# Optimization experiments

Measured on AMD Instinct MI355X. Metric: run time of the kernel, lower is better.

Reference implementation:

```python
import math
import jax, jax.numpy as jnp
import numpy as np

B, N, C, H = 64, 197, 768, 12
KEEP_RATE = 0.7

def setup_inputs() -> dict:
    key = jax.random.key(0)
    k0, k1, k2 = jax.random.split(key, 3)
    x = jax.random.normal(k0, (B, N, C), jnp.float32)
    qkv_w = jax.random.normal(k1, (C, 3 * C), jnp.float32) * 0.02
    qkv_b = jnp.zeros((3 * C,), jnp.float32)
    proj_w = jax.random.normal(k2, (C, C), jnp.float32) * 0.02
    proj_b = jnp.zeros((C,), jnp.float32)
    return {"x": x, "qkv_w": qkv_w, "qkv_b": qkv_b, "proj_w": proj_w, "proj_b": proj_b}

def reference(x, qkv_w, qkv_b, proj_w, proj_b):
    b, n, c = x.shape
    d = c // H
    scale = d ** -0.5
    # qkv: [B,N,3C] -> [3,B,H,N,d]
    qkv = (x @ qkv_w + qkv_b).reshape(b, n, 3, H, d)
    qkv = jnp.transpose(qkv, (2, 0, 3, 1, 4))
    q, k, v = qkv[0], qkv[1], qkv[2]
    attn = jax.nn.softmax(jnp.einsum('bhnd,bhmd->bhnm', q, k) * scale, axis=-1)  # [B,H,N,N]
    out = jnp.einsum('bhnm,bhmd->bhnd', attn, v)          # [B,H,N,d]
    out = jnp.transpose(out, (0, 2, 1, 3)).reshape(b, n, c)
    x_out = out @ proj_w + proj_b                          # [B,N,C]
    # dynamic token pruning via CLS attention (row 0, excluding CLS itself)
    left_tokens = math.ceil(KEEP_RATE * (n - 1))
    cls_attn = attn[:, :, 0, 1:].mean(axis=1)              # [B,N-1]
    _, idx = jax.lax.top_k(cls_attn, left_tokens)          # descending, sorted
    index = jnp.broadcast_to(idx[:, :, None], (b, left_tokens, c))
    return (x_out, index, idx, cls_attn, left_tokens)
```

## Files before the change

kernel.cpp:

```cpp
#include <hip/hip_runtime.h>
#include <math.h>

#define BB   64
#define NTOK 197
#define CC   768
#define HH   12
#define DH   64
#define MTOT (BB * NTOK)
#define MPAD 12672
#define LEFT 138

#define XOUT_OFF  0
#define INDEX_OFF 9682944
#define IDX_OFF   16465920
#define CLS_OFF   16474752
#define LT_OFF    16487296

typedef short s8v __attribute__((ext_vector_type(8)));
typedef short s4v __attribute__((ext_vector_type(4)));
typedef float f4v __attribute__((ext_vector_type(4)));

#define GLOAD16(g, l) __builtin_amdgcn_global_load_lds( \
    (const __attribute__((address_space(1))) unsigned int*)(g), \
    (__attribute__((address_space(3))) unsigned int*)(l), 16, 0, 0)

__device__ __forceinline__ unsigned short f2bf(float f) {
    union { float f; unsigned int i; } x; x.f = f;
    unsigned int r = x.i + 0x7FFFu + ((x.i >> 16) & 1u);
    return (unsigned short)(r >> 16);
}

__global__ __launch_bounds__(256)
void convert_x(const float* __restrict__ in, unsigned short* __restrict__ outb)
{
    size_t i = ((size_t)blockIdx.x * 256 + threadIdx.x) * 8;
    float4 a = *(const float4*)(in + i);
    float4 b = *(const float4*)(in + i + 4);
    s8v r;
    r[0] = (short)f2bf(a.x); r[1] = (short)f2bf(a.y);
    r[2] = (short)f2bf(a.z); r[3] = (short)f2bf(a.w);
    r[4] = (short)f2bf(b.x); r[5] = (short)f2bf(b.y);
    r[6] = (short)f2bf(b.z); r[7] = (short)f2bf(b.w);
    *(s8v*)(outb + i) = r;
}

__global__ __launch_bounds__(256)
void transpose_w2(const float* __restrict__ inq, const float* __restrict__ inp,
                  unsigned short* __restrict__ outq, unsigned short* __restrict__ outp)
{
    __shared__ float tile[32][33];
    const int bi = blockIdx.x;
    int bj = blockIdx.y;
    const float* in; unsigned short* outb; int N;
    if (bj < 72) { in = inq; outb = outq; N = 2304; }
    else         { bj -= 72; in = inp; outb = outp; N = 768; }
    const int tx = threadIdx.x & 31, ty = threadIdx.x >> 5;
#pragma unroll
    for (int r = ty; r < 32; r += 8)
        tile[r][tx] = in[(size_t)(bi * 32 + r) * N + bj * 32 + tx];
    __syncthreads();
#pragma unroll
    for (int r = ty; r < 32; r += 8)
        outb[(size_t)(bj * 32 + r) * 768 + bi * 32 + tx] = f2bf(tile[tx][r]);
}

__global__ __launch_bounds__(256, 3)
void gemm_bf16(const unsigned short* __restrict__ A, const unsigned short* __restrict__ BT,
               const float* __restrict__ bias, int ncolt, int mode,
               unsigned short* __restrict__ outb, float* __restrict__ outf)
{
    const int id = blockIdx.x;
    const int xcd = id & 7;
    const int t = id >> 3;
    const int ct = t % ncolt, s = t / ncolt;
    const int rt = s * 8 + xcd;
    if (rt >= 99) return;
    const int m0 = rt * 128, n0 = ct * 128;

    const int tid = threadIdx.x;
    const int wave = tid >> 6, lane = tid & 63;
    const int quad = lane >> 4, l16 = lane & 15;
    const int rowbase = (wave >> 1) * 64, colbase = (wave & 1) * 64;
    __shared__ __align__(16) short As[128 * 64];
    __shared__ __align__(16) short Bs[128 * 64];

    const int rA   = lane >> 3;
    const int gcol = ((lane & 7) ^ rA) * 8;
    unsigned int agof[4], bgof[4];
#pragma unroll
    for (int i = 0; i < 4; ++i) {
        int c = wave * 4 + i;
        agof[i] = (unsigned int)((m0 + c * 8 + rA) * 768 + gcol);
        bgof[i] = (unsigned int)((n0 + c * 8 + rA) * 768 + gcol);
    }
    int aoff[4], boff[4];
#pragma unroll
    for (int i = 0; i < 4; ++i) {
        aoff[i] = (rowbase + i * 16 + l16) * 64 + ((quad ^ (l16 & 7)) * 8);
        boff[i] = (colbase + i * 16 + l16) * 64 + ((quad ^ (l16 & 7)) * 8);
    }

    f4v acc[4][4];
#pragma unroll
    for (int i = 0; i < 4; ++i)
#pragma unroll
        for (int j = 0; j < 4; ++j) acc[i][j] = (f4v)0.f;

    for (int k0 = 0; k0 < 768; k0 += 64) {
#pragma unroll
        for (int i = 0; i < 4; ++i) {
            int c = wave * 4 + i;
            GLOAD16(A  + agof[i] + k0, &As[c * 512]);
            GLOAD16(BT + bgof[i] + k0, &Bs[c * 512]);
        }
        __syncthreads();
#pragma unroll
        for (int ks = 0; ks < 2; ++ks) {
            const int x = ks * 32;
            s8v af[4], bf[4];
#pragma unroll
            for (int i = 0; i < 4; ++i) af[i] = *(const s8v*)&As[aoff[i] ^ x];
#pragma unroll
            for (int j = 0; j < 4; ++j) bf[j] = *(const s8v*)&Bs[boff[j] ^ x];
#pragma unroll
            for (int i = 0; i < 4; ++i)
#pragma unroll
                for (int j = 0; j < 4; ++j)
                    acc[i][j] = __builtin_amdgcn_mfma_f32_16x16x32_bf16(bf[j], af[i], acc[i][j], 0, 0, 0);
        }
        __syncthreads();
    }

    const int ncols = mode ? 768 : 2304;
#pragma unroll
    for (int i = 0; i < 4; ++i) {
        const int m = m0 + rowbase + i * 16 + l16;
        if (m >= MTOT) continue;
#pragma unroll
        for (int j = 0; j < 4; ++j) {
            const int nb = n0 + colbase + j * 16 + quad * 4;
            float4 b4 = *(const float4*)&bias[nb];
            if (mode == 1) {
                float4 r;
                r.x = acc[i][j][0] + b4.x; r.y = acc[i][j][1] + b4.y;
                r.z = acc[i][j][2] + b4.z; r.w = acc[i][j][3] + b4.w;
                *(float4*)(outf + (size_t)m * ncols + nb) = r;
            } else {
                s4v r;
                r[0] = (short)f2bf(acc[i][j][0] + b4.x);
                r[1] = (short)f2bf(acc[i][j][1] + b4.y);
                r[2] = (short)f2bf(acc[i][j][2] + b4.z);
                r[3] = (short)f2bf(acc[i][j][3] + b4.w);
                *(s4v*)(outb + (size_t)m * ncols + nb) = r;
            }
        }
    }
}

#define PSTR 226
#define AW   5
#define ATH  320

__global__ __launch_bounds__(ATH)
void attn_mfma(const unsigned short* __restrict__ qkv, unsigned short* __restrict__ attnbf)
{
    const int bh = blockIdx.x;
    const int b = bh / HH, h = bh - b * HH;
    const int tid = threadIdx.x;
    const int wave = tid >> 6, lane = tid & 63;
    const int quad = lane >> 4, l16 = lane & 15;
    __shared__ short Vs[64 * PSTR];
    __shared__ short Ps[AW][16 * PSTR];

    const unsigned short* qg = qkv + (size_t)b * NTOK * 2304 + h * DH;
    const unsigned short* kg = qg + 768;
    const unsigned short* vg = qg + 1536;

    if (tid < NTOK) {
#pragma unroll
        for (int c = 0; c < 8; ++c) {
            s8v vv = *(const s8v*)(vg + (size_t)tid * 2304 + c * 8);
#pragma unroll
            for (int e = 0; e < 8; ++e) Vs[(c * 8 + e) * PSTR + tid] = vv[e];
        }
    }
    for (int f = tid; f < 64 * (PSTR - NTOK); f += ATH) {
        int dd = f / (PSTR - NTOK);
        int tk = NTOK + (f - dd * (PSTR - NTOK));
        Vs[dd * PSTR + tk] = 0;
    }
    __syncthreads();

    for (int strip = wave; strip < 13; strip += AW) {
        const int mq = min(strip * 16 + l16, NTOK - 1);
        const s8v aq0 = *(const s8v*)(qg + (size_t)mq * 2304 + quad * 8);
        const s8v aq1 = *(const s8v*)(qg + (size_t)mq * 2304 + 32 + quad * 8);

        f4v sacc[14];
#pragma unroll
        for (int j = 0; j < 14; ++j) sacc[j] = (f4v)0.f;
        __builtin_amdgcn_s_setprio(1);
#pragma unroll
        for (int j = 0; j < 14; ++j) {
            const int kt = min(j * 16 + l16, NTOK - 1);
            s8v bk0 = *(const s8v*)(kg + (size_t)kt * 2304 + quad * 8);
            s8v bk1 = *(const s8v*)(kg + (size_t)kt * 2304 + 32 + quad * 8);
            sacc[j] = __builtin_amdgcn_mfma_f32_16x16x32_bf16(bk0, aq0, sacc[j], 0, 0, 0);
            sacc[j] = __builtin_amdgcn_mfma_f32_16x16x32_bf16(bk1, aq1, sacc[j], 0, 0, 0);
        }
        __builtin_amdgcn_s_setprio(0);

        float mx = -1e30f;
#pragma unroll
        for (int j = 0; j < 14; ++j)
#pragma unroll
            for (int r = 0; r < 4; ++r) {
                const int key = j * 16 + quad * 4 + r;
                float s = (key < NTOK) ? sacc[j][r] * 0.125f : -1e30f;
                sacc[j][r] = s;
                mx = fmaxf(mx, s);
            }
        mx = fmaxf(mx, __shfl_xor(mx, 16, 64));
        mx = fmaxf(mx, __shfl_xor(mx, 32, 64));

        float sm = 0.f;
#pragma unroll
        for (int j = 0; j < 14; ++j) {
            s4v pk;
#pragma unroll
            for (int r = 0; r < 4; ++r) {
                const int key = j * 16 + quad * 4 + r;
                float p = (key < NTOK) ? __expf(sacc[j][r] - mx) : 0.f;
                sm += p;
                pk[r] = (short)f2bf(p);
            }
            *(s4v*)&Ps[wave][l16 * PSTR + j * 16 + quad * 4] = pk;
        }
        sm += __shfl_xor(sm, 16, 64);
        sm += __shfl_xor(sm, 32, 64);
        const float rcp = 1.f / sm;

        f4v oacc[4];
#pragma unroll
        for (int j = 0; j < 4; ++j) oacc[j] = (f4v)0.f;
        __builtin_amdgcn_s_setprio(1);
#pragma unroll
        for (int t = 0; t < 7; ++t) {
            const int ko = t * 32 + quad * 8;
            s8v ap = *(const s8v*)&Ps[wave][l16 * PSTR + ko];
#pragma unroll
            for (int j = 0; j < 4; ++j) {
                s8v bv = *(const s8v*)&Vs[(j * 16 + l16) * PSTR + ko];
                oacc[j] = __builtin_amdgcn_mfma_f32_16x16x32_bf16(bv, ap, oacc[j], 0, 0, 0);
            }
        }
        __builtin_amdgcn_s_setprio(0);
        const int qrow = strip * 16 + l16;
        if (qrow < NTOK) {
#pragma unroll
            for (int j = 0; j < 4; ++j) {
                s4v o4;
#pragma unroll
                for (int r = 0; r < 4; ++r) o4[r] = (short)f2bf(oacc[j][r] * rcp);
                *(s4v*)&attnbf[((size_t)b * NTOK + qrow) * 768 + h * DH + j * 16 + quad * 4] = o4;
            }
        }
    }
}

#define QCH  64
#define BGRP 8

__global__ __launch_bounds__(256)
void qr_kernel(const float* __restrict__ x, const float* __restrict__ qkv_w,
               const float* __restrict__ qkv_b, float* __restrict__ rws,
               float* __restrict__ bconst)
{
    const int h  = blockIdx.x;
    const int b0 = blockIdx.y * BGRP;
    const int tid = threadIdx.x;
    __shared__ float x0s[BGRP][CC];
    __shared__ float wbuf[2][QCH * DH];
    __shared__ float q0s[BGRP][DH];

    for (int u = tid; u < BGRP * CC; u += 256) {
        int b = u / CC, c = u - b * CC;
        x0s[b][c] = x[(size_t)(b0 + b) * NTOK * CC + c];
    }
    for (int u = tid; u < QCH * DH; u += 256) {
        int cc = u >> 6, dd = u & 63;
        wbuf[0][u] = qkv_w[(size_t)cc * 2304 + h * DH + dd];
    }
    __syncthreads();

    const int d  = tid & 63;
    const int bA = tid >> 6;
    const int bB = bA + 4;
    float accA = qkv_b[h * DH + d];
    float accB = qkv_b[h * DH + d];
    for (int k = 0; k < CC / QCH; ++k) {
        const int cur = k & 1;
        if (k + 1 < CC / QCH) {
            const int cbase = (k + 1) * QCH;
            for (int u = tid; u < QCH * DH; u += 256) {
                int cc = u >> 6, dd = u & 63;
                wbuf[cur ^ 1][u] = qkv_w[(size_t)(cbase + cc) * 2304 + h * DH + dd];
            }
        }
        const int cb = k * QCH;
#pragma unroll
        for (int cc = 0; cc < QCH; ++cc) {
            const float wv = wbuf[cur][cc * 64 + d];
            accA = fmaf(x0s[bA][cb + cc], wv, accA);
            accB = fmaf(x0s[bB][cb + cc], wv, accB);
        }
        __syncthreads();
    }
    q0s[bA][d] = accA;
    q0s[bB][d] = accB;
    __syncthreads();

    if (tid < BGRP) {
        float acc3 = 0.f;
        for (int dd = 0; dd < DH; ++dd) acc3 += q0s[tid][dd] * qkv_b[CC + h * DH + dd];
        bconst[(b0 + tid) * HH + h] = acc3;
    }

    for (int c = tid; c < CC; c += 256) {
        const float* wrow = qkv_w + (size_t)c * 2304 + CC + h * DH;
        float acc2[BGRP];
#pragma unroll
        for (int b = 0; b < BGRP; ++b) acc2[b] = 0.f;
#pragma unroll
        for (int dd = 0; dd < DH; dd += 4) {
            float4 w4 = *(const float4*)(wrow + dd);
#pragma unroll
            for (int b = 0; b < BGRP; ++b) {
                acc2[b] = fmaf(w4.x, q0s[b][dd + 0], acc2[b]);
                acc2[b] = fmaf(w4.y, q0s[b][dd + 1], acc2[b]);
                acc2[b] = fmaf(w4.z, q0s[b][dd + 2], acc2[b]);
                acc2[b] = fmaf(w4.w, q0s[b][dd + 3], acc2[b]);
            }
        }
#pragma unroll
        for (int b = 0; b < BGRP; ++b)
            rws[((size_t)(b0 + b) * HH + h) * CC + c] = acc2[b];
    }
}

__global__ __launch_bounds__(256)
void cls_s(const float* __restrict__ x, const float* __restrict__ rws,
           const float* __restrict__ bconst, float* __restrict__ sws)
{
    const int b = blockIdx.y;
    const int tid = threadIdx.x;
    __shared__ __align__(16) float rl[HH * 772];
    __shared__ float bcs[HH];
#pragma unroll
    for (int h = 0; h < HH; ++h)
        for (int c = tid; c < CC; c += 256)
            rl[h * 772 + c] = rws[((size_t)b * HH + h) * CC + c];
    if (tid < HH) bcs[tid] = bconst[b * HH + tid];
    __syncthreads();
    const int local = blockIdx.x * 256 + tid;
    if (local < NTOK * HH) {
        const int tok = local / HH;
        const int h = local - tok * HH;
        const float* xr = x + ((size_t)b * NTOK + tok) * CC;
        const float* rp = rl + h * 772;
        float acc = 0.f;
#pragma unroll 8
        for (int c = 0; c < CC; c += 4) {
            float4 x4 = *(const float4*)(xr + c);
            float4 r4 = *(const float4*)(rp + c);
            acc = fmaf(x4.x, r4.x, acc);
            acc = fmaf(x4.y, r4.y, acc);
            acc = fmaf(x4.z, r4.z, acc);
            acc = fmaf(x4.w, r4.w, acc);
        }
        sws[((size_t)b * HH + h) * NTOK + tok] = (acc + bcs[h]) * 0.125f;
    }
}

__global__ __launch_bounds__(256)
void cls_topk(const float* __restrict__ sws, float* __restrict__ out, int write_lt)
{
    const int b = blockIdx.x, tid = threadIdx.x;
    const int wave = tid >> 6, lane = tid & 63;
    __shared__ float sbuf[HH][208];
    __shared__ float pm[4][208];
    __shared__ float vals[256];
    __shared__ int   idxs[256];

    for (int jj = lane; jj < 208; jj += 64) pm[wave][jj] = 0.f;
    if (tid < NTOK) {
#pragma unroll
        for (int h = 0; h < HH; ++h)
            sbuf[h][tid] = sws[((size_t)b * HH + h) * NTOK + tid];
    }
    __syncthreads();

    for (int h = wave; h < HH; h += 4) {
        float sv[4], ev[4];
        float mx = -1e30f;
#pragma unroll
        for (int t = 0; t < 4; ++t) {
            int j = lane + 64 * t;
            sv[t] = (j < NTOK) ? sbuf[h][j] : -1e30f;
            mx = fmaxf(mx, sv[t]);
        }
#pragma unroll
        for (int off = 1; off < 64; off <<= 1) mx = fmaxf(mx, __shfl_xor(mx, off, 64));
        float sm = 0.f;
#pragma unroll
        for (int t = 0; t < 4; ++t) {
            int j = lane + 64 * t;
            ev[t] = (j < NTOK) ? expf(sv[t] - mx) : 0.f;
            sm += ev[t];
        }
#pragma unroll
        for (int off = 1; off < 64; off <<= 1) sm += __shfl_xor(sm, off, 64);
#pragma unroll
        for (int t = 0; t < 4; ++t) {
            int j = lane + 64 * t;
            if (j < NTOK) pm[wave][j] += ev[t] / sm;
        }
    }
    __syncthreads();

    float v = -INFINITY;
    int id = 256 + tid;
    if (tid < NTOK - 1) {
        int j = tid + 1;
        float s = ((pm[0][j] + pm[1][j]) + (pm[2][j] + pm[3][j])) * (1.f / 12.f);
        v = s; id = tid;
        out[CLS_OFF + (size_t)b * (NTOK - 1) + tid] = s;
    }
    vals[tid] = v; idxs[tid] = id;
    __syncthreads();

    for (int k = 2; k <= 256; k <<= 1) {
        for (int j = k >> 1; j > 0; j >>= 1) {
            int ixj = tid ^ j;
            if (ixj > tid) {
                float va = vals[tid], vb2 = vals[ixj];
                int ia = idxs[tid], ib = idxs[ixj];
                bool aLess = (va > vb2) || (va == vb2 && ia < ib);
                bool dir = ((tid & k) == 0);
                if (dir != aLess) {
                    vals[tid] = vb2; vals[ixj] = va;
                    idxs[tid] = ib;  idxs[ixj] = ia;
                }
            }
            __syncthreads();
        }
    }

    if (tid < LEFT) out[IDX_OFF + (size_t)b * LEFT + tid] = (float)idxs[tid];
    if (write_lt && b == 0 && tid == 0) out[LT_OFF] = (float)LEFT;
}

__global__ __launch_bounds__(64)
void write_index(const float* __restrict__ idx_in, float* __restrict__ out)
{
    const int row = blockIdx.x;
    const float v = idx_in[row];
    const int tid = threadIdx.x;
    float4 r; r.x = v; r.y = v; r.z = v; r.w = v;
#pragma unroll
    for (int i = 0; i < 3; ++i)
        *(float4*)(out + INDEX_OFF + (size_t)row * CC + (tid + 64 * i) * 4) = r;
}

extern "C" void kernel_launch(void* const* d_in, const int* in_sizes, int n_in,
                              void* d_out, int out_size, void* d_ws, size_t ws_size,
                              hipStream_t stream)
{
    const float* x      = (const float*)d_in[0];
    const float* qkv_w  = (const float*)d_in[1];
    const float* qkv_b  = (const float*)d_in[2];
    const float* proj_w = (const float*)d_in[3];
    const float* proj_b = (const float*)d_in[4];
    float* out = (float*)d_out;

    char* w = (char*)d_ws;
    unsigned short* xbf   = (unsigned short*)w; w += (size_t)MPAD * CC * 2;
    unsigned short* wt1   = (unsigned short*)w; w += (size_t)3 * CC * CC * 2;
    unsigned short* wt2   = (unsigned short*)w; w += (size_t)CC * CC * 2;
    unsigned short* qkvbf = (unsigned short*)w; w += (size_t)MTOT * 3 * CC * 2;
    unsigned short* atbf  = (unsigned short*)w; w += (size_t)MPAD * CC * 2;
    float* rws    = (float*)w; w += (size_t)BB * HH * CC * 4;
    float* bconst = (float*)w; w += (size_t)BB * HH * 4;
    float* sws    = (float*)w; w += (size_t)BB * HH * NTOK * 4;

    convert_x<<<dim3(4728), 256, 0, stream>>>(x, xbf);
    transpose_w2<<<dim3(24, 96), 256, 0, stream>>>(qkv_w, proj_w, wt1, wt2);
    qr_kernel<<<dim3(HH, BB / BGRP), 256, 0, stream>>>(x, qkv_w, qkv_b, rws, bconst);
    cls_s<<<dim3(10, 64), 256, 0, stream>>>(x, rws, bconst, sws);
    cls_topk<<<dim3(BB), 256, 0, stream>>>(sws, out, (out_size > LT_OFF) ? 1 : 0);
    write_index<<<dim3(BB * LEFT), 64, 0, stream>>>(out + IDX_OFF, out);
    for (int part = 0; part < 3; ++part)
        gemm_bf16<<<dim3(8 * 6 * 13), 256, 0, stream>>>(
            xbf, wt1 + (size_t)part * 768 * 768, qkv_b + part * 768, 6, 0,
            qkvbf + part * 768, nullptr);
    attn_mfma<<<dim3(BB * HH), ATH, 0, stream>>>(qkvbf, atbf);
    gemm_bf16<<<dim3(8 * 6 * 13), 256, 0, stream>>>(atbf, wt2, proj_b, 6, 1,
                                                    nullptr, out + XOUT_OFF);
}
```

Measured before the change: 355.7 us.

## Fuse QKV GEMM launches and pre-transpose V for attention

```diff
diff --git a/kernel.cpp b/kernel.cpp
--- a/kernel.cpp
+++ b/kernel.cpp
@@ -157,39 +157,49 @@
     }
 }
 
+#define VTS 224
+
+__global__ __launch_bounds__(256)
+void transpose_v(const unsigned short* __restrict__ qkv, unsigned short* __restrict__ vt)
+{
+    __shared__ short tile[32][33];
+    const int bx = blockIdx.x;
+    const int by = blockIdx.y;
+    const int bh = blockIdx.z;
+    const int b = bh / HH, h = bh - b * HH;
+    const int tx = threadIdx.x & 31, ty = threadIdx.x >> 5;
+    const unsigned short* vin = qkv + (size_t)b * NTOK * 2304 + 1536 + h * DH;
+#pragma unroll
+    for (int r = ty; r < 32; r += 8) {
+        const int tok = bx * 32 + r;
+        tile[r][tx] = (tok < NTOK) ? (short)vin[(size_t)tok * 2304 + by * 32 + tx] : (short)0;
+    }
+    __syncthreads();
+#pragma unroll
+    for (int r = ty; r < 32; r += 8) {
+        const int d = by * 32 + r;
+        vt[((size_t)bh * DH + d) * VTS + bx * 32 + tx] = tile[tx][r];
+    }
+}
+
 #define PSTR 226
 #define AW   5
 #define ATH  320
 
 __global__ __launch_bounds__(ATH)
-void attn_mfma(const unsigned short* __restrict__ qkv, unsigned short* __restrict__ attnbf)
+void attn_mfma(const unsigned short* __restrict__ qkv, const unsigned short* __restrict__ vt,
+               unsigned short* __restrict__ attnbf)
 {
     const int bh = blockIdx.x;
     const int b = bh / HH, h = bh - b * HH;
     const int tid = threadIdx.x;
     const int wave = tid >> 6, lane = tid & 63;
     const int quad = lane >> 4, l16 = lane & 15;
-    __shared__ short Vs[64 * PSTR];
     __shared__ short Ps[AW][16 * PSTR];
 
     const unsigned short* qg = qkv + (size_t)b * NTOK * 2304 + h * DH;
     const unsigned short* kg = qg + 768;
-    const unsigned short* vg = qg + 1536;
-
-    if (tid < NTOK) {
-#pragma unroll
-        for (int c = 0; c < 8; ++c) {
-            s8v vv = *(const s8v*)(vg + (size_t)tid * 2304 + c * 8);
-#pragma unroll
-            for (int e = 0; e < 8; ++e) Vs[(c * 8 + e) * PSTR + tid] = vv[e];
-        }
-    }
-    for (int f = tid; f < 64 * (PSTR - NTOK); f += ATH) {
-        int dd = f / (PSTR - NTOK);
-        int tk = NTOK + (f - dd * (PSTR - NTOK));
-        Vs[dd * PSTR + tk] = 0;
-    }
-    __syncthreads();
+    const unsigned short* vtb = vt + (size_t)bh * DH * VTS;
 
     for (int strip = wave; strip < 13; strip += AW) {
         const int mq = min(strip * 16 + l16, NTOK - 1);
@@ -250,7 +260,7 @@
             s8v ap = *(const s8v*)&Ps[wave][l16 * PSTR + ko];
 #pragma unroll
             for (int j = 0; j < 4; ++j) {
-                s8v bv = *(const s8v*)&Vs[(j * 16 + l16) * PSTR + ko];
+                s8v bv = *(const s8v*)(vtb + (size_t)(j * 16 + l16) * VTS + ko);
                 oacc[j] = __builtin_amdgcn_mfma_f32_16x16x32_bf16(bv, ap, oacc[j], 0, 0, 0);
             }
         }
@@ -492,6 +502,7 @@
     float* rws    = (float*)w; w += (size_t)BB * HH * CC * 4;
     float* bconst = (float*)w; w += (size_t)BB * HH * 4;
     float* sws    = (float*)w; w += (size_t)BB * HH * NTOK * 4;
+    unsigned short* vtbf  = (unsigned short*)d_ws;
 
     convert_x<<<dim3(4728), 256, 0, stream>>>(x, xbf);
     transpose_w2<<<dim3(24, 96), 256, 0, stream>>>(qkv_w, proj_w, wt1, wt2);
@@ -499,11 +510,9 @@
     cls_s<<<dim3(10, 64), 256, 0, stream>>>(x, rws, bconst, sws);
     cls_topk<<<dim3(BB), 256, 0, stream>>>(sws, out, (out_size > LT_OFF) ? 1 : 0);
     write_index<<<dim3(BB * LEFT), 64, 0, stream>>>(out + IDX_OFF, out);
-    for (int part = 0; part < 3; ++part)
-        gemm_bf16<<<dim3(8 * 6 * 13), 256, 0, stream>>>(
-            xbf, wt1 + (size_t)part * 768 * 768, qkv_b + part * 768, 6, 0,
-            qkvbf + part * 768, nullptr);
-    attn_mfma<<<dim3(BB * HH), ATH, 0, stream>>>(qkvbf, atbf);
+    gemm_bf16<<<dim3(8 * 18 * 13), 256, 0, stream>>>(xbf, wt1, qkv_b, 18, 0, qkvbf, nullptr);
+    transpose_v<<<dim3(7, 2, BB * HH), 256, 0, stream>>>(qkvbf, vtbf);
+    attn_mfma<<<dim3(BB * HH), ATH, 0, stream>>>(qkvbf, vtbf, atbf);
     gemm_bf16<<<dim3(8 * 6 * 13), 256, 0, stream>>>(atbf, wt2, proj_b, 6, 1,
                                                     nullptr, out + XOUT_OFF);
 }
```

Measured after the change: 363.5 us. +2.2%, slower.
